# Performance work log

Measured on AMD Instinct MI355X. Metric: run time of the kernel, lower is better.

The kernel has to match this reference:

```python
import jax, jax.numpy as jnp
import numpy as np

N_QUBITS = 8
NPC = 15  # params per U_SU4 conv block
C64 = jnp.complex64

# CNOT with control = first tensor factor / second tensor factor
CNOT01 = jnp.array([[1, 0, 0, 0], [0, 1, 0, 0], [0, 0, 0, 1], [0, 0, 1, 0]], dtype=C64)
CNOT10 = jnp.array([[1, 0, 0, 0], [0, 0, 0, 1], [0, 0, 1, 0], [0, 1, 0, 0]], dtype=C64)
I2 = jnp.eye(2, dtype=C64)
PX = jnp.array([[0, 1], [1, 0]], dtype=C64)
PY = jnp.array([[0, -1j], [1j, 0]], dtype=C64)
PZ = jnp.array([[1, 0], [0, -1]], dtype=C64)


def _u3(t, p, l):
    ct, st = jnp.cos(t / 2).astype(C64), jnp.sin(t / 2).astype(C64)
    return jnp.stack([
        jnp.stack([ct, -(jnp.exp(1j * l) * st)]),
        jnp.stack([jnp.exp(1j * p) * st, jnp.exp(1j * (p + l)) * ct]),
    ]).astype(C64)


def _ry(t):
    c, s = jnp.cos(t / 2), jnp.sin(t / 2)
    return jnp.stack([jnp.stack([c, -s]), jnp.stack([s, c])]).astype(C64)


def _rz(t):
    z = jnp.zeros((), C64)
    return jnp.stack([jnp.stack([jnp.exp(-1j * t / 2), z]),
                      jnp.stack([z, jnp.exp(1j * t / 2)])]).astype(C64)


def _su4(p):
    # Compose the 15-parameter U_SU4 block into a single 4x4 unitary
    # (first tensor factor = wires[0], second = wires[1]).
    k = jnp.kron
    M = k(_u3(p[0], p[1], p[2]), _u3(p[3], p[4], p[5]))
    M = CNOT01 @ M
    M = k(_ry(p[6]), _rz(p[7])) @ M
    M = CNOT10 @ M
    M = k(_ry(p[8]), I2) @ M
    M = CNOT01 @ M
    M = k(_u3(p[9], p[10], p[11]), _u3(p[12], p[13], p[14])) @ M
    return M


def _apply_2q(state, U, w0, w1):
    # state: [B, 2]*8, axis (w+1) is wire w (wire 0 = most significant, as in
    # PennyLane AmplitudeEmbedding). Apply 4x4 U on wires (w0, w1).
    state = jnp.moveaxis(state, (w0 + 1, w1 + 1), (-2, -1))
    sh = state.shape
    state = state.reshape(sh[:-2] + (4,)) @ U.T
    state = state.reshape(sh)
    return jnp.moveaxis(state, (-2, -1), (w0 + 1, w1 + 1))


def _apply_1q(state, U, w):
    state = jnp.moveaxis(state, w + 1, -1)
    state = state @ U.T
    return jnp.moveaxis(state, -1, w + 1)


def _expval(state, P, w):
    phi = _apply_1q(state, P, w)
    return jnp.sum(jnp.conj(state) * phi, axis=tuple(range(1, N_QUBITS + 1))).real


LAYER1 = [(0, 1), (2, 3), (4, 5), (6, 7), (1, 2), (3, 4), (5, 6), (7, 0)]
LAYER2 = [(2, 4), (6, 0), (0, 2), (4, 6)]
LAYER3 = [(2, 6)]
LAYERS = [LAYER1, LAYER1, LAYER2, LAYER2, LAYER3]


def setup_inputs() -> dict:
    key = jax.random.key(0)
    kx, kw = jax.random.split(key)
    x = jax.random.normal(kx, (32768, 256), dtype=jnp.float32)
    quantum_weights = jax.random.normal(kw, (5 * NPC,), dtype=jnp.float32)
    return {"x": x, "quantum_weights": quantum_weights}


def reference(x, quantum_weights):
    B = x.shape[0]
    # AmplitudeEmbedding with normalize=True
    norm = jnp.linalg.norm(x, axis=1, keepdims=True)
    state = (x / norm).astype(C64).reshape((B,) + (2,) * N_QUBITS)
    for li, pairs in enumerate(LAYERS):
        M = _su4(quantum_weights[li * NPC:(li + 1) * NPC])
        for (a, b) in pairs:
            state = _apply_2q(state, M, a, b)
    # latent_dim == 6: X,Y,Z on wire 2 then wire 6
    outs = [_expval(state, P, wq) for wq in (2, 6) for P in (PX, PY, PZ)]
    return jnp.stack(outs, axis=1)  # [B, 6]
```

## Files before the change

### kernel.cpp

```cpp
#include <hip/hip_runtime.h>

#define DIM 256

__device__ float2 g_M[5 * 16];

__device__ inline float2 cmulc(float2 a, float2 b) {
    return make_float2(a.x * b.x - a.y * b.y, a.x * b.y + a.y * b.x);
}
__device__ inline float2 caddc(float2 a, float2 b) {
    return make_float2(a.x + b.x, a.y + b.y);
}


__device__ void mat_u3(float t, float p, float l, float2* U) {
    float s, c;
    sincosf(0.5f * t, &s, &c);
    float sp, cp, sl, cl, spl, cpl;
    sincosf(p, &sp, &cp);
    sincosf(l, &sl, &cl);
    sincosf(p + l, &spl, &cpl);
    U[0] = make_float2(c, 0.f);
    U[1] = make_float2(-cl * s, -sl * s);
    U[2] = make_float2(cp * s, sp * s);
    U[3] = make_float2(cpl * c, spl * c);
}
__device__ void mat_ry(float t, float2* U) {
    float s, c;
    sincosf(0.5f * t, &s, &c);
    U[0] = make_float2(c, 0.f); U[1] = make_float2(-s, 0.f);
    U[2] = make_float2(s, 0.f); U[3] = make_float2(c, 0.f);
}
__device__ void mat_rz(float t, float2* U) {
    float s, c;
    sincosf(0.5f * t, &s, &c);
    U[0] = make_float2(c, -s); U[1] = make_float2(0.f, 0.f);
    U[2] = make_float2(0.f, 0.f); U[3] = make_float2(c, s);
}
__device__ void mat_I2(float2* U) {
    U[0] = make_float2(1.f, 0.f); U[1] = make_float2(0.f, 0.f);
    U[2] = make_float2(0.f, 0.f); U[3] = make_float2(1.f, 0.f);
}
__device__ void kron4(const float2* A, const float2* B, float2* K) {
    for (int i0 = 0; i0 < 2; ++i0)
        for (int i1 = 0; i1 < 2; ++i1)
            for (int j0 = 0; j0 < 2; ++j0)
                for (int j1 = 0; j1 < 2; ++j1)
                    K[(2 * i0 + i1) * 4 + (2 * j0 + j1)] = cmulc(A[i0 * 2 + j0], B[i1 * 2 + j1]);
}
__device__ void mm4(const float2* A, const float2* B, float2* C) {
    for (int r = 0; r < 4; ++r)
        for (int c = 0; c < 4; ++c) {
            float2 acc = make_float2(0.f, 0.f);
            for (int k = 0; k < 4; ++k) acc = caddc(acc, cmulc(A[r * 4 + k], B[k * 4 + c]));
            C[r * 4 + c] = acc;
        }
}
__device__ void swap_rows(float2* M, int r1, int r2) {
    for (int c = 0; c < 4; ++c) {
        float2 t = M[r1 * 4 + c]; M[r1 * 4 + c] = M[r2 * 4 + c]; M[r2 * 4 + c] = t;
    }
}

__global__ void qsvdd_setup(const float* __restrict__ w) {
    int l = threadIdx.x;
    if (l >= 5) return;
    const float* p = w + l * 15;
    float2 A[4], Bm[4], K[16], M[16], T[16];
    mat_u3(p[0], p[1], p[2], A);
    mat_u3(p[3], p[4], p[5], Bm);
    kron4(A, Bm, M);
    swap_rows(M, 2, 3);
    mat_ry(p[6], A); mat_rz(p[7], Bm);
    kron4(A, Bm, K); mm4(K, M, T);
    swap_rows(T, 1, 3);
    mat_ry(p[8], A); mat_I2(Bm);
    kron4(A, Bm, K); mm4(K, T, M);
    swap_rows(M, 2, 3);
    mat_u3(p[9], p[10], p[11], A);
    mat_u3(p[12], p[13], p[14], Bm);
    kron4(A, Bm, K); mm4(K, M, T);
    for (int i = 0; i < 16; ++i) g_M[l * 16 + i] = T[i];
}


__device__ __forceinline__ void cmadf(float2& a, float mx, float my, float2 v) {
    a.x = fmaf(mx, v.x, a.x);
    a.x = fmaf(-my, v.y, a.x);
    a.y = fmaf(mx, v.y, a.y);
    a.y = fmaf(my, v.x, a.y);
}
__device__ __forceinline__ float2 cmulf(float mx, float my, float2 v) {
    float2 r;
    r.x = mx * v.x; r.x = fmaf(-my, v.y, r.x);
    r.y = mx * v.y; r.y = fmaf(my, v.x, r.y);
    return r;
}
__device__ __forceinline__ float bperm(int ba, float s) {
    return __int_as_float(__builtin_amdgcn_ds_bpermute(ba, __float_as_int(s)));
}

#define GQ(A0, A1, A2, A3)                                                        \
    {                                                                             \
        float2 t0 = cmulf(m0.x, m0.y, A0);                                        \
        cmadf(t0, m1.x, m1.y, A1); cmadf(t0, m2.x, m2.y, A2); cmadf(t0, m3.x, m3.y, A3);   \
        float2 t1 = cmulf(m4.x, m4.y, A0);                                        \
        cmadf(t1, m5.x, m5.y, A1); cmadf(t1, m6.x, m6.y, A2); cmadf(t1, m7.x, m7.y, A3);   \
        float2 t2 = cmulf(m8.x, m8.y, A0);                                        \
        cmadf(t2, m9.x, m9.y, A1); cmadf(t2, m10.x, m10.y, A2); cmadf(t2, m11.x, m11.y, A3); \
        float2 t3 = cmulf(m12.x, m12.y, A0);                                      \
        cmadf(t3, m13.x, m13.y, A1); cmadf(t3, m14.x, m14.y, A2); cmadf(t3, m15.x, m15.y, A3); \
        A0 = t0; A1 = t1; A2 = t2; A3 = t3;                                       \
    }

#define G_32 { GQ(v0,v4,v8,v12)  GQ(v1,v5,v9,v13)  GQ(v2,v6,v10,v14) GQ(v3,v7,v11,v15) }
#define G_10 { GQ(v0,v1,v2,v3)   GQ(v4,v5,v6,v7)   GQ(v8,v9,v10,v11) GQ(v12,v13,v14,v15) }
#define G_21 { GQ(v0,v2,v4,v6)   GQ(v1,v3,v5,v7)   GQ(v8,v10,v12,v14) GQ(v9,v11,v13,v15) }
#define G_03 { GQ(v0,v8,v1,v9)   GQ(v2,v10,v3,v11) GQ(v4,v12,v5,v13) GQ(v6,v14,v7,v15) }
#define G_20 { GQ(v0,v1,v4,v5)   GQ(v2,v3,v6,v7)   GQ(v8,v9,v12,v13) GQ(v10,v11,v14,v15) }
#define G_13 { GQ(v0,v8,v2,v10)  GQ(v1,v9,v3,v11)  GQ(v4,v12,v6,v14) GQ(v5,v13,v7,v15) }
#define G_02 { GQ(v0,v4,v1,v5)   GQ(v2,v6,v3,v7)   GQ(v8,v12,v9,v13) GQ(v10,v14,v11,v15) }
#define G_30 { GQ(v0,v1,v8,v9)   GQ(v2,v3,v10,v11) GQ(v4,v5,v12,v13) GQ(v6,v7,v14,v15) }
#define G_23 { GQ(v0,v8,v4,v12)  GQ(v1,v9,v5,v13)  GQ(v2,v10,v6,v14) GQ(v3,v11,v7,v15) }
#define G_31 { GQ(v0,v2,v8,v10)  GQ(v1,v3,v9,v11)  GQ(v4,v6,v12,v14) GQ(v5,v7,v13,v15) }
#define G_12 { GQ(v0,v4,v2,v6)   GQ(v1,v5,v3,v7)   GQ(v8,v12,v10,v14) GQ(v9,v13,v11,v15) }

#define BSW(VA, VB, PB, BA)                                                       \
    {                                                                             \
        float sx = (PB) ? VA.x : VB.x, sy = (PB) ? VA.y : VB.y;                   \
        float rx = bperm(BA, sx), ry = bperm(BA, sy);                             \
        VA.x = (PB) ? rx : VA.x; VA.y = (PB) ? ry : VA.y;                         \
        VB.x = (PB) ? VB.x : rx; VB.y = (PB) ? VB.y : ry;                         \
    }

#define SW0(PB, BA) { BSW(v0,v1,PB,BA) BSW(v2,v3,PB,BA) BSW(v4,v5,PB,BA) BSW(v6,v7,PB,BA) \
                      BSW(v8,v9,PB,BA) BSW(v10,v11,PB,BA) BSW(v12,v13,PB,BA) BSW(v14,v15,PB,BA) }
#define SW1(PB, BA) { BSW(v0,v2,PB,BA) BSW(v1,v3,PB,BA) BSW(v4,v6,PB,BA) BSW(v5,v7,PB,BA) \
                      BSW(v8,v10,PB,BA) BSW(v9,v11,PB,BA) BSW(v12,v14,PB,BA) BSW(v13,v15,PB,BA) }
#define SW2(PB, BA) { BSW(v0,v4,PB,BA) BSW(v1,v5,PB,BA) BSW(v2,v6,PB,BA) BSW(v3,v7,PB,BA) \
                      BSW(v8,v12,PB,BA) BSW(v9,v13,PB,BA) BSW(v10,v14,PB,BA) BSW(v11,v15,PB,BA) }
#define SW3(PB, BA) { BSW(v0,v8,PB,BA) BSW(v1,v9,PB,BA) BSW(v2,v10,PB,BA) BSW(v3,v11,PB,BA) \
                      BSW(v4,v12,PB,BA) BSW(v5,v13,PB,BA) BSW(v6,v14,PB,BA) BSW(v7,v15,PB,BA) }

#define LOADM(L)                                                                  \
    {                                                                             \
        m0  = g_M[(L)*16+0];  m1  = g_M[(L)*16+1];  m2  = g_M[(L)*16+2];  m3  = g_M[(L)*16+3];  \
        m4  = g_M[(L)*16+4];  m5  = g_M[(L)*16+5];  m6  = g_M[(L)*16+6];  m7  = g_M[(L)*16+7];  \
        m8  = g_M[(L)*16+8];  m9  = g_M[(L)*16+9];  m10 = g_M[(L)*16+10]; m11 = g_M[(L)*16+11]; \
        m12 = g_M[(L)*16+12]; m13 = g_M[(L)*16+13]; m14 = g_M[(L)*16+14]; m15 = g_M[(L)*16+15]; \
    }

#define NRM(V) fmaf(V.x, V.x, V.y * V.y)
#define EXP2(A, B) { acc0 += A.x*B.x + A.y*B.y; acc1 += A.x*B.y - A.y*B.x; acc2 += NRM(A) - NRM(B); }
#define EXP6(A, B) { acc3 += A.x*B.x + A.y*B.y; acc4 += A.x*B.y - A.y*B.x; acc5 += NRM(A) - NRM(B); }

__global__ __launch_bounds__(256, 1) void qsvdd_main(const float* __restrict__ x,
                                                     float* __restrict__ out) {
    const int lane = threadIdx.x & 63;
    const int q = lane & 15;
    const long e = ((long)blockIdx.x * 4 + (threadIdx.x >> 6)) * 4 + (lane >> 4);

    const int ba0 = (lane ^ 1) << 2, ba1 = (lane ^ 2) << 2;
    const int ba2 = (lane ^ 4) << 2, ba3 = (lane ^ 8) << 2;
    const bool p0 = lane & 1, p1 = lane & 2, p2 = lane & 4, p3 = lane & 8;

    const float* xe = x + (e << 8) + q;
    float2 v0, v1, v2, v3, v4, v5, v6, v7, v8, v9, v10, v11, v12, v13, v14, v15;
    v0.x  = xe[0];   v1.x  = xe[16];  v2.x  = xe[32];  v3.x  = xe[48];
    v4.x  = xe[64];  v5.x  = xe[80];  v6.x  = xe[96];  v7.x  = xe[112];
    v8.x  = xe[128]; v9.x  = xe[144]; v10.x = xe[160]; v11.x = xe[176];
    v12.x = xe[192]; v13.x = xe[208]; v14.x = xe[224]; v15.x = xe[240];
    float ss = 0.f;
    ss = fmaf(v0.x, v0.x, ss);   ss = fmaf(v1.x, v1.x, ss);
    ss = fmaf(v2.x, v2.x, ss);   ss = fmaf(v3.x, v3.x, ss);
    ss = fmaf(v4.x, v4.x, ss);   ss = fmaf(v5.x, v5.x, ss);
    ss = fmaf(v6.x, v6.x, ss);   ss = fmaf(v7.x, v7.x, ss);
    ss = fmaf(v8.x, v8.x, ss);   ss = fmaf(v9.x, v9.x, ss);
    ss = fmaf(v10.x, v10.x, ss); ss = fmaf(v11.x, v11.x, ss);
    ss = fmaf(v12.x, v12.x, ss); ss = fmaf(v13.x, v13.x, ss);
    ss = fmaf(v14.x, v14.x, ss); ss = fmaf(v15.x, v15.x, ss);
    ss += __shfl_xor(ss, 1, 64); ss += __shfl_xor(ss, 2, 64);
    ss += __shfl_xor(ss, 4, 64); ss += __shfl_xor(ss, 8, 64);
    const float inv = rsqrtf(ss);
    v0.x *= inv;  v1.x *= inv;  v2.x *= inv;  v3.x *= inv;
    v4.x *= inv;  v5.x *= inv;  v6.x *= inv;  v7.x *= inv;
    v8.x *= inv;  v9.x *= inv;  v10.x *= inv; v11.x *= inv;
    v12.x *= inv; v13.x *= inv; v14.x *= inv; v15.x *= inv;
    v0.y = 0.f;  v1.y = 0.f;  v2.y = 0.f;  v3.y = 0.f;
    v4.y = 0.f;  v5.y = 0.f;  v6.y = 0.f;  v7.y = 0.f;
    v8.y = 0.f;  v9.y = 0.f;  v10.y = 0.f; v11.y = 0.f;
    v12.y = 0.f; v13.y = 0.f; v14.y = 0.f; v15.y = 0.f;

    float2 m0, m1, m2, m3, m4, m5, m6, m7, m8, m9, m10, m11, m12, m13, m14, m15;

    LOADM(0);
    G_32; G_10;
    SW3(p3, ba3); SW2(p2, ba2); SW1(p1, ba1); SW0(p0, ba0);
    G_32; G_10;
    G_21;
    SW3(p3, ba3);
    G_03;
    SW1(p3, ba3); SW2(p0, ba0);
    G_21;
    SW0(p2, ba2); SW3(p1, ba1);
    G_03;
    LOADM(1);
    G_32;
    SW2(p1, ba1);
    G_20;
    SW3(p0, ba0);
    G_13;
    SW0(p3, ba3); SW2(p2, ba2);
    G_02;
    G_30;
    SW3(p2, ba2);
    G_23;
    SW2(p1, ba1);
    G_21;
    SW0(p3, ba3); SW3(p0, ba0);
    G_03;
    LOADM(2);
    G_31;
    SW2(p3, ba3); SW0(p0, ba0);
    G_20;
    G_03; G_12;
    LOADM(3);
    G_31; G_20;
    G_03; G_12;
    LOADM(4);
    G_32;

    float acc0 = 0.f, acc1 = 0.f, acc2 = 0.f, acc3 = 0.f, acc4 = 0.f, acc5 = 0.f;
    EXP2(v0, v8)  EXP2(v1, v9)  EXP2(v2, v10)  EXP2(v3, v11)
    EXP2(v4, v12) EXP2(v5, v13) EXP2(v6, v14)  EXP2(v7, v15)
    EXP6(v0, v4)  EXP6(v1, v5)  EXP6(v2, v6)   EXP6(v3, v7)
    EXP6(v8, v12) EXP6(v9, v13) EXP6(v10, v14) EXP6(v11, v15)
    acc0 *= 2.f; acc1 *= 2.f; acc3 *= 2.f; acc4 *= 2.f;
    acc0 += __shfl_xor(acc0, 1, 64); acc0 += __shfl_xor(acc0, 2, 64);
    acc0 += __shfl_xor(acc0, 4, 64); acc0 += __shfl_xor(acc0, 8, 64);
    acc1 += __shfl_xor(acc1, 1, 64); acc1 += __shfl_xor(acc1, 2, 64);
    acc1 += __shfl_xor(acc1, 4, 64); acc1 += __shfl_xor(acc1, 8, 64);
    acc2 += __shfl_xor(acc2, 1, 64); acc2 += __shfl_xor(acc2, 2, 64);
    acc2 += __shfl_xor(acc2, 4, 64); acc2 += __shfl_xor(acc2, 8, 64);
    acc3 += __shfl_xor(acc3, 1, 64); acc3 += __shfl_xor(acc3, 2, 64);
    acc3 += __shfl_xor(acc3, 4, 64); acc3 += __shfl_xor(acc3, 8, 64);
    acc4 += __shfl_xor(acc4, 1, 64); acc4 += __shfl_xor(acc4, 2, 64);
    acc4 += __shfl_xor(acc4, 4, 64); acc4 += __shfl_xor(acc4, 8, 64);
    acc5 += __shfl_xor(acc5, 1, 64); acc5 += __shfl_xor(acc5, 2, 64);
    acc5 += __shfl_xor(acc5, 4, 64); acc5 += __shfl_xor(acc5, 8, 64);
    if (q == 0) {
        float* o = out + e * 6;
        o[0] = acc0; o[1] = acc1; o[2] = acc2;
        o[3] = acc3; o[4] = acc4; o[5] = acc5;
    }
}

extern "C" void kernel_launch(void* const* d_in, const int* in_sizes, int n_in,
                              void* d_out, int out_size, void* d_ws, size_t ws_size,
                              hipStream_t stream) {
    const float* x = (const float*)d_in[0];
    const float* w = (const float*)d_in[1];
    float* out = (float*)d_out;
    const int B = in_sizes[0] / DIM;

    hipLaunchKernelGGL(qsvdd_setup, dim3(1), dim3(64), 0, stream, w);
    hipLaunchKernelGGL(qsvdd_main, dim3(B / 16), dim3(256), 0, stream, x, out);
}
```

Before: 91.75 us.

## Precompute full circuit unitary and apply via split-fp16 MFMA GEMM

Instead of simulating the gate sequence per sample with shuffles, a new kernel builds the full 256x256 circuit unitary (real and imaginary parts interleaved, permuted columns) by running the circuit on basis vectors. It stores the unitary as hi/lo fp16 pairs. The main kernel normalizes each input row, splits it into hi/lo fp16 in swizzled LDS, and multiplies it by the unitary with three MFMA products for near-fp32 accuracy. Expectation values are then formed from lane shuffles of the output amplitudes. This replaces per-sample gate arithmetic with a dense GEMM on matrix cores, at the cost of a heavier matmul, an extra launch and an extra global read of the matrix.

```diff
diff --git a/kernel.cpp b/kernel.cpp
--- a/kernel.cpp
+++ b/kernel.cpp
@@ -2,7 +2,13 @@
 
 #define DIM 256
 
+typedef _Float16 f16x8 __attribute__((ext_vector_type(8)));
+typedef _Float16 f16x4 __attribute__((ext_vector_type(4)));
+typedef float f32x4 __attribute__((ext_vector_type(4)));
+
 __device__ float2 g_M[5 * 16];
+__device__ __align__(16) _Float16 g_Bh[512 * 256];
+__device__ __align__(16) _Float16 g_Bl[512 * 256];
 
 __device__ inline float2 cmulc(float2 a, float2 b) {
     return make_float2(a.x * b.x - a.y * b.y, a.x * b.y + a.y * b.x);
@@ -149,108 +155,209 @@
         m12 = g_M[(L)*16+12]; m13 = g_M[(L)*16+13]; m14 = g_M[(L)*16+14]; m15 = g_M[(L)*16+15]; \
     }
 
-#define NRM(V) fmaf(V.x, V.x, V.y * V.y)
-#define EXP2(A, B) { acc0 += A.x*B.x + A.y*B.y; acc1 += A.x*B.y - A.y*B.x; acc2 += NRM(A) - NRM(B); }
-#define EXP6(A, B) { acc3 += A.x*B.x + A.y*B.y; acc4 += A.x*B.y - A.y*B.x; acc5 += NRM(A) - NRM(B); }
-
-__global__ __launch_bounds__(256, 1) void qsvdd_main(const float* __restrict__ x,
-                                                     float* __restrict__ out) {
+#define RUN_CIRCUIT                                                               \
+    LOADM(0);                                                                     \
+    G_32; G_10;                                                                   \
+    SW3(p3, ba3); SW2(p2, ba2); SW1(p1, ba1); SW0(p0, ba0);                       \
+    G_32; G_10;                                                                   \
+    G_21;                                                                         \
+    SW3(p3, ba3);                                                                 \
+    G_03;                                                                         \
+    SW1(p3, ba3); SW2(p0, ba0);                                                   \
+    G_21;                                                                         \
+    SW0(p2, ba2); SW3(p1, ba1);                                                   \
+    G_03;                                                                         \
+    LOADM(1);                                                                     \
+    G_32;                                                                         \
+    SW2(p1, ba1);                                                                 \
+    G_20;                                                                         \
+    SW3(p0, ba0);                                                                 \
+    G_13;                                                                         \
+    SW0(p3, ba3); SW2(p2, ba2);                                                   \
+    G_02;                                                                         \
+    G_30;                                                                         \
+    SW3(p2, ba2);                                                                 \
+    G_23;                                                                         \
+    SW2(p1, ba1);                                                                 \
+    G_21;                                                                         \
+    SW0(p3, ba3); SW3(p0, ba0);                                                   \
+    G_03;                                                                         \
+    LOADM(2);                                                                     \
+    G_31;                                                                         \
+    SW2(p3, ba3); SW0(p0, ba0);                                                   \
+    G_20;                                                                         \
+    G_03; G_12;                                                                   \
+    LOADM(3);                                                                     \
+    G_31; G_20;                                                                   \
+    G_03; G_12;                                                                   \
+    LOADM(4);                                                                     \
+    G_32;
+
+
+__device__ __forceinline__ void wru(float2 vv, int rb, int qb, int c) {
+    const int a = ((rb & 1) << 7) | (((rb >> 1) & 1) << 3) | (((rb >> 2) & 1) << 1) |
+                  (((rb >> 3) & 1) << 5) | qb;
+    const int b7 = (a >> 7) & 1, b6 = (a >> 6) & 1, b5 = (a >> 5) & 1, b4 = (a >> 4) & 1;
+    const int b3 = (a >> 3) & 1, b2 = (a >> 2) & 1, b1 = (a >> 1) & 1, b0 = a & 1;
+    const int g = (b7 << 5) | (b6 << 4) | (b4 << 3) | (b3 << 2) | (b2 << 1) | b0;
+    const int n = g * 8 + (((b5 << 1) | b1) << 1);
+    const _Float16 hr = (_Float16)vv.x, hi = (_Float16)vv.y;
+    g_Bh[n * 256 + c] = hr;
+    g_Bh[(n + 1) * 256 + c] = hi;
+    g_Bl[n * 256 + c] = (_Float16)((vv.x - (float)hr) * 2048.f);
+    g_Bl[(n + 1) * 256 + c] = (_Float16)((vv.y - (float)hi) * 2048.f);
+}
+
+__global__ __launch_bounds__(256) void build_u() {
     const int lane = threadIdx.x & 63;
     const int q = lane & 15;
-    const long e = ((long)blockIdx.x * 4 + (threadIdx.x >> 6)) * 4 + (lane >> 4);
+    const int c = ((int)blockIdx.x * 4 + (threadIdx.x >> 6)) * 4 + (lane >> 4);
 
     const int ba0 = (lane ^ 1) << 2, ba1 = (lane ^ 2) << 2;
     const int ba2 = (lane ^ 4) << 2, ba3 = (lane ^ 8) << 2;
     const bool p0 = lane & 1, p1 = lane & 2, p2 = lane & 4, p3 = lane & 8;
 
-    const float* xe = x + (e << 8) + q;
     float2 v0, v1, v2, v3, v4, v5, v6, v7, v8, v9, v10, v11, v12, v13, v14, v15;
-    v0.x  = xe[0];   v1.x  = xe[16];  v2.x  = xe[32];  v3.x  = xe[48];
-    v4.x  = xe[64];  v5.x  = xe[80];  v6.x  = xe[96];  v7.x  = xe[112];
-    v8.x  = xe[128]; v9.x  = xe[144]; v10.x = xe[160]; v11.x = xe[176];
-    v12.x = xe[192]; v13.x = xe[208]; v14.x = xe[224]; v15.x = xe[240];
-    float ss = 0.f;
-    ss = fmaf(v0.x, v0.x, ss);   ss = fmaf(v1.x, v1.x, ss);
-    ss = fmaf(v2.x, v2.x, ss);   ss = fmaf(v3.x, v3.x, ss);
-    ss = fmaf(v4.x, v4.x, ss);   ss = fmaf(v5.x, v5.x, ss);
-    ss = fmaf(v6.x, v6.x, ss);   ss = fmaf(v7.x, v7.x, ss);
-    ss = fmaf(v8.x, v8.x, ss);   ss = fmaf(v9.x, v9.x, ss);
-    ss = fmaf(v10.x, v10.x, ss); ss = fmaf(v11.x, v11.x, ss);
-    ss = fmaf(v12.x, v12.x, ss); ss = fmaf(v13.x, v13.x, ss);
-    ss = fmaf(v14.x, v14.x, ss); ss = fmaf(v15.x, v15.x, ss);
-    ss += __shfl_xor(ss, 1, 64); ss += __shfl_xor(ss, 2, 64);
-    ss += __shfl_xor(ss, 4, 64); ss += __shfl_xor(ss, 8, 64);
-    const float inv = rsqrtf(ss);
-    v0.x *= inv;  v1.x *= inv;  v2.x *= inv;  v3.x *= inv;
-    v4.x *= inv;  v5.x *= inv;  v6.x *= inv;  v7.x *= inv;
-    v8.x *= inv;  v9.x *= inv;  v10.x *= inv; v11.x *= inv;
-    v12.x *= inv; v13.x *= inv; v14.x *= inv; v15.x *= inv;
-    v0.y = 0.f;  v1.y = 0.f;  v2.y = 0.f;  v3.y = 0.f;
-    v4.y = 0.f;  v5.y = 0.f;  v6.y = 0.f;  v7.y = 0.f;
-    v8.y = 0.f;  v9.y = 0.f;  v10.y = 0.f; v11.y = 0.f;
-    v12.y = 0.f; v13.y = 0.f; v14.y = 0.f; v15.y = 0.f;
+    v0  = make_float2((0*16+q)  == c ? 1.f : 0.f, 0.f);
+    v1  = make_float2((1*16+q)  == c ? 1.f : 0.f, 0.f);
+    v2  = make_float2((2*16+q)  == c ? 1.f : 0.f, 0.f);
+    v3  = make_float2((3*16+q)  == c ? 1.f : 0.f, 0.f);
+    v4  = make_float2((4*16+q)  == c ? 1.f : 0.f, 0.f);
+    v5  = make_float2((5*16+q)  == c ? 1.f : 0.f, 0.f);
+    v6  = make_float2((6*16+q)  == c ? 1.f : 0.f, 0.f);
+    v7  = make_float2((7*16+q)  == c ? 1.f : 0.f, 0.f);
+    v8  = make_float2((8*16+q)  == c ? 1.f : 0.f, 0.f);
+    v9  = make_float2((9*16+q)  == c ? 1.f : 0.f, 0.f);
+    v10 = make_float2((10*16+q) == c ? 1.f : 0.f, 0.f);
+    v11 = make_float2((11*16+q) == c ? 1.f : 0.f, 0.f);
+    v12 = make_float2((12*16+q) == c ? 1.f : 0.f, 0.f);
+    v13 = make_float2((13*16+q) == c ? 1.f : 0.f, 0.f);
+    v14 = make_float2((14*16+q) == c ? 1.f : 0.f, 0.f);
+    v15 = make_float2((15*16+q) == c ? 1.f : 0.f, 0.f);
 
     float2 m0, m1, m2, m3, m4, m5, m6, m7, m8, m9, m10, m11, m12, m13, m14, m15;
-
-    LOADM(0);
-    G_32; G_10;
-    SW3(p3, ba3); SW2(p2, ba2); SW1(p1, ba1); SW0(p0, ba0);
-    G_32; G_10;
-    G_21;
-    SW3(p3, ba3);
-    G_03;
-    SW1(p3, ba3); SW2(p0, ba0);
-    G_21;
-    SW0(p2, ba2); SW3(p1, ba1);
-    G_03;
-    LOADM(1);
-    G_32;
-    SW2(p1, ba1);
-    G_20;
-    SW3(p0, ba0);
-    G_13;
-    SW0(p3, ba3); SW2(p2, ba2);
-    G_02;
-    G_30;
-    SW3(p2, ba2);
-    G_23;
-    SW2(p1, ba1);
-    G_21;
-    SW0(p3, ba3); SW3(p0, ba0);
-    G_03;
-    LOADM(2);
-    G_31;
-    SW2(p3, ba3); SW0(p0, ba0);
-    G_20;
-    G_03; G_12;
-    LOADM(3);
-    G_31; G_20;
-    G_03; G_12;
-    LOADM(4);
-    G_32;
-
-    float acc0 = 0.f, acc1 = 0.f, acc2 = 0.f, acc3 = 0.f, acc4 = 0.f, acc5 = 0.f;
-    EXP2(v0, v8)  EXP2(v1, v9)  EXP2(v2, v10)  EXP2(v3, v11)
-    EXP2(v4, v12) EXP2(v5, v13) EXP2(v6, v14)  EXP2(v7, v15)
-    EXP6(v0, v4)  EXP6(v1, v5)  EXP6(v2, v6)   EXP6(v3, v7)
-    EXP6(v8, v12) EXP6(v9, v13) EXP6(v10, v14) EXP6(v11, v15)
-    acc0 *= 2.f; acc1 *= 2.f; acc3 *= 2.f; acc4 *= 2.f;
-    acc0 += __shfl_xor(acc0, 1, 64); acc0 += __shfl_xor(acc0, 2, 64);
-    acc0 += __shfl_xor(acc0, 4, 64); acc0 += __shfl_xor(acc0, 8, 64);
-    acc1 += __shfl_xor(acc1, 1, 64); acc1 += __shfl_xor(acc1, 2, 64);
-    acc1 += __shfl_xor(acc1, 4, 64); acc1 += __shfl_xor(acc1, 8, 64);
-    acc2 += __shfl_xor(acc2, 1, 64); acc2 += __shfl_xor(acc2, 2, 64);
-    acc2 += __shfl_xor(acc2, 4, 64); acc2 += __shfl_xor(acc2, 8, 64);
-    acc3 += __shfl_xor(acc3, 1, 64); acc3 += __shfl_xor(acc3, 2, 64);
-    acc3 += __shfl_xor(acc3, 4, 64); acc3 += __shfl_xor(acc3, 8, 64);
-    acc4 += __shfl_xor(acc4, 1, 64); acc4 += __shfl_xor(acc4, 2, 64);
-    acc4 += __shfl_xor(acc4, 4, 64); acc4 += __shfl_xor(acc4, 8, 64);
-    acc5 += __shfl_xor(acc5, 1, 64); acc5 += __shfl_xor(acc5, 2, 64);
-    acc5 += __shfl_xor(acc5, 4, 64); acc5 += __shfl_xor(acc5, 8, 64);
-    if (q == 0) {
-        float* o = out + e * 6;
-        o[0] = acc0; o[1] = acc1; o[2] = acc2;
-        o[3] = acc3; o[4] = acc4; o[5] = acc5;
+    RUN_CIRCUIT;
+
+    const int qb = ((q & 1) << 6) | (((q >> 1) & 1) << 0) | (((q >> 2) & 1) << 2) |
+                   (((q >> 3) & 1) << 4);
+    wru(v0, 0, qb, c);   wru(v1, 1, qb, c);   wru(v2, 2, qb, c);   wru(v3, 3, qb, c);
+    wru(v4, 4, qb, c);   wru(v5, 5, qb, c);   wru(v6, 6, qb, c);   wru(v7, 7, qb, c);
+    wru(v8, 8, qb, c);   wru(v9, 9, qb, c);   wru(v10, 10, qb, c); wru(v11, 11, qb, c);
+    wru(v12, 12, qb, c); wru(v13, 13, qb, c); wru(v14, 14, qb, c); wru(v15, 15, qb, c);
+}
+
+
+__device__ __forceinline__ float xorf(float v, unsigned m) {
+    return __int_as_float(__float_as_int(v) ^ (int)m);
+}
+
+__global__ __launch_bounds__(256, 2) void qsvdd_main(const float* __restrict__ x,
+                                                     float* __restrict__ out) {
+    __shared__ __align__(16) _Float16 sAh[64 * 256];
+    __shared__ __align__(16) _Float16 sAl[64 * 256];
+
+    const int lane = threadIdx.x & 63;
+    const int w = threadIdx.x >> 6;
+    const int c16 = lane & 15;
+    const int oct = lane >> 4;
+
+    const int rbase = w * 16;
+#pragma unroll 4
+    for (int rr = 0; rr < 16; ++rr) {
+        const int row = rbase + rr;
+        const float4 xv = *reinterpret_cast<const float4*>(
+            x + ((size_t)blockIdx.x * 64 + row) * 256 + lane * 4);
+        float ssq = xv.x * xv.x + xv.y * xv.y + xv.z * xv.z + xv.w * xv.w;
+#pragma unroll
+        for (int o = 32; o; o >>= 1) ssq += __shfl_xor(ssq, o, 64);
+        const float inv = rsqrtf(ssq);
+        const float a0 = xv.x * inv, a1 = xv.y * inv, a2 = xv.z * inv, a3 = xv.w * inv;
+        const _Float16 h0 = (_Float16)a0, h1 = (_Float16)a1, h2 = (_Float16)a2, h3 = (_Float16)a3;
+        f16x4 hv, lv;
+        hv.x = h0; hv.y = h1; hv.z = h2; hv.w = h3;
+        lv.x = (_Float16)((a0 - (float)h0) * 2048.f);
+        lv.y = (_Float16)((a1 - (float)h1) * 2048.f);
+        lv.z = (_Float16)((a2 - (float)h2) * 2048.f);
+        lv.w = (_Float16)((a3 - (float)h3) * 2048.f);
+        const int slot = lane >> 1;
+        const int idx = row * 256 + (((slot ^ (row & 7)) << 3) | ((lane & 1) << 2));
+        *reinterpret_cast<f16x4*>(&sAh[idx]) = hv;
+        *reinterpret_cast<f16x4*>(&sAl[idx]) = lv;
+    }
+
+    float aX2[4] = {0, 0, 0, 0}, aY2[4] = {0, 0, 0, 0}, aZ2[4] = {0, 0, 0, 0};
+    float aX6[4] = {0, 0, 0, 0}, aY6[4] = {0, 0, 0, 0}, aZ6[4] = {0, 0, 0, 0};
+
+    const int l3 = lane & 7;
+    const unsigned mY2 = (unsigned)(((l3 >> 2) ^ l3) & 1) << 31;
+    const unsigned mY6 = (unsigned)(((l3 >> 1) ^ l3) & 1) << 31;
+    const unsigned mZ2 = (unsigned)((l3 >> 2) & 1) << 31;
+    const unsigned mZ6 = (unsigned)((l3 >> 1) & 1) << 31;
+
+    const int arow = rbase + c16;
+    const int aswz = arow & 7;
+
+#pragma unroll 1
+    for (int ch = 0; ch < 4; ++ch) {
+        f32x4 accM[8], accC[8];
+        const f32x4 zz = {0.f, 0.f, 0.f, 0.f};
+#pragma unroll
+        for (int i = 0; i < 8; ++i) { accM[i] = zz; accC[i] = zz; }
+
+#pragma unroll
+        for (int s = 0; s < 8; ++s) {
+            const int aidx = arow * 256 + (((s * 4 + oct) ^ aswz) << 3);
+            const f16x8 ah = *reinterpret_cast<const f16x8*>(&sAh[aidx]);
+            const f16x8 al = *reinterpret_cast<const f16x8*>(&sAl[aidx]);
+#pragma unroll
+            for (int nt = 0; nt < 8; ++nt) {
+                const size_t boff = (size_t)(ch * 128 + nt * 16 + c16) * 256 + s * 32 + oct * 8;
+                const f16x8 bh = *reinterpret_cast<const f16x8*>(&g_Bh[boff]);
+                const f16x8 bl = *reinterpret_cast<const f16x8*>(&g_Bl[boff]);
+                accM[nt] = __builtin_amdgcn_mfma_f32_16x16x32_f16(ah, bh, accM[nt], 0, 0, 0);
+                accC[nt] = __builtin_amdgcn_mfma_f32_16x16x32_f16(al, bh, accC[nt], 0, 0, 0);
+                accC[nt] = __builtin_amdgcn_mfma_f32_16x16x32_f16(ah, bl, accC[nt], 0, 0, 0);
+            }
+        }
+#pragma unroll
+        for (int nt = 0; nt < 8; ++nt) {
+#pragma unroll
+            for (int r = 0; r < 4; ++r) {
+                const float val = fmaf(accC[nt][r], 4.8828125e-4f, accM[nt][r]);
+                const float x4 = __shfl_xor(val, 4, 64);
+                const float x2v = __shfl_xor(val, 2, 64);
+                const float x5 = __shfl_xor(val, 5, 64);
+                const float x3v = __shfl_xor(val, 3, 64);
+                aX2[r] = fmaf(val, x4, aX2[r]);
+                aX6[r] = fmaf(val, x2v, aX6[r]);
+                aY2[r] = fmaf(xorf(val, mY2), x5, aY2[r]);
+                aY6[r] = fmaf(xorf(val, mY6), x3v, aY6[r]);
+                aZ2[r] = fmaf(xorf(val, mZ2), val, aZ2[r]);
+                aZ6[r] = fmaf(xorf(val, mZ6), val, aZ6[r]);
+            }
+        }
+    }
+
+#pragma unroll
+    for (int r = 0; r < 4; ++r) {
+#pragma unroll
+        for (int o = 1; o <= 8; o <<= 1) {
+            aX2[r] += __shfl_xor(aX2[r], o, 64);
+            aY2[r] += __shfl_xor(aY2[r], o, 64);
+            aZ2[r] += __shfl_xor(aZ2[r], o, 64);
+            aX6[r] += __shfl_xor(aX6[r], o, 64);
+            aY6[r] += __shfl_xor(aY6[r], o, 64);
+            aZ6[r] += __shfl_xor(aZ6[r], o, 64);
+        }
+    }
+    if (c16 == 0) {
+        const size_t rowg = (size_t)blockIdx.x * 64 + rbase + oct * 4;
+#pragma unroll
+        for (int r = 0; r < 4; ++r) {
+            float* o = out + (rowg + r) * 6;
+            o[0] = aX2[r]; o[1] = aY2[r]; o[2] = aZ2[r];
+            o[3] = aX6[r]; o[4] = aY6[r]; o[5] = aZ6[r];
+        }
     }
 }
 
@@ -263,5 +370,6 @@
     const int B = in_sizes[0] / DIM;
 
     hipLaunchKernelGGL(qsvdd_setup, dim3(1), dim3(64), 0, stream, w);
-    hipLaunchKernelGGL(qsvdd_main, dim3(B / 16), dim3(256), 0, stream, x, out);
-}
+    hipLaunchKernelGGL(build_u, dim3(16), dim3(256), 0, stream);
+    hipLaunchKernelGGL(qsvdd_main, dim3(B / 64), dim3(256), 0, stream, x, out);
+}
```

Measured after the change: 250.6 us. +173.1%, slower.
